# Kernel tuning notes

Hardware: AMD Instinct MI355X
Metric: run time of the kernel (lower is better)

The kernel has to match this reference:

```python
import jax, jax.numpy as jnp
import numpy as np

H = 4        # num_heads
KNN = 10     # k_knn neighbors gathered by distance
KS = 4       # k_select top-k neighbors kept by attention score
EPS = 1e-5
BIG = 1e9


def _ln(x, g, b):
    m = x.mean(-1, keepdims=True)
    v = ((x - m) ** 2).mean(-1, keepdims=True)
    return (x - m) * jax.lax.rsqrt(v + EPS) * g + b


def _sparse_dyn_voxel_attn(x, coords, mask, w_qkv, b_qkv, w_proj, b_proj):
    # x: [B,N,C], coords: [B,N,3], mask: [B,N] bool
    B, N, C = x.shape
    dh = C // H
    qkv = x @ w_qkv + b_qkv                       # [B,N,3C]
    q, k, v = jnp.split(qkv, 3, axis=-1)
    q = q.reshape(B, N, H, dh).transpose(0, 2, 1, 3)   # [B,H,N,dh]
    k = k.reshape(B, N, H, dh).transpose(0, 2, 1, 3)
    v = v.reshape(B, N, H, dh).transpose(0, 2, 1, 3)

    # KNN over voxel coordinates; empty voxels pushed to far distance
    d2 = jnp.sum((coords[:, :, None, :] - coords[:, None, :, :]) ** 2, axis=-1)  # [B,N,N]
    d2 = jnp.where(mask[:, None, :], d2, BIG)
    _, nbr = jax.lax.top_k(-d2, KNN)              # [B,N,KNN] nearest-neighbor indices

    # gather neighbor keys/values: [B,H,N,KNN,dh]
    kn = jax.vmap(lambda a, i: a[:, i, :])(k, nbr)
    vn = jax.vmap(lambda a, i: a[:, i, :])(v, nbr)
    nmask = jax.vmap(lambda m, i: m[i])(mask, nbr)  # [B,N,KNN]

    scale = float(1.0 / np.sqrt(dh))
    scores = jnp.einsum('bhnd,bhnkd->bhnk', q, kn) * scale  # [B,H,N,KNN]
    scores = scores + jnp.where(nmask, 0.0, -BIG)[:, None, :, :]

    # dynamic selection: keep top k_select neighbors by score, softmax over them
    sv, si = jax.lax.top_k(scores, KS)            # [B,H,N,KS]
    w = jax.nn.softmax(sv, axis=-1)
    vsel = jnp.take_along_axis(vn, si[..., None], axis=3)   # [B,H,N,KS,dh]
    o = jnp.einsum('bhnk,bhnkd->bhnd', w, vsel)   # [B,H,N,dh]
    o = o.transpose(0, 2, 1, 3).reshape(B, N, C) @ w_proj + b_proj
    return jnp.where(mask[..., None], o, 0.0)


def setup_inputs() -> dict:
    key = jax.random.key(0)
    ks = jax.random.split(key, 8)
    B, N, C, M = 4, 4096, 64, 256  # N = 16^3 voxels
    s = lambda k, sh: jax.random.normal(k, sh, jnp.float32) * 0.02
    return dict(
        inputs=jax.random.normal(ks[0], (B, N, C), jnp.float32),
        voxel_coords=jax.random.uniform(ks[1], (B, N, 3), jnp.float32) * 16.0,
        non_empty_mask=jax.random.randint(ks[2], (B, N), 0, 2).astype(bool),
        ln1_g=jnp.ones(C, jnp.float32), ln1_b=jnp.zeros(C, jnp.float32),
        ln2_g=jnp.ones(C, jnp.float32), ln2_b=jnp.zeros(C, jnp.float32),
        w_qkv=s(ks[3], (C, 3 * C)), b_qkv=jnp.zeros(3 * C, jnp.float32),
        w_proj=s(ks[4], (C, C)), b_proj=jnp.zeros(C, jnp.float32),
        w1=s(ks[5], (C, M)), b1=jnp.zeros(M, jnp.float32),
        w2=s(ks[6], (M, C)), b2=jnp.zeros(C, jnp.float32),
    )


def reference(inputs, voxel_coords, non_empty_mask, ln1_g, ln1_b, ln2_g, ln2_b,
              w_qkv, b_qkv, w_proj, b_proj, w1, b1, w2, b2):
    a = _sparse_dyn_voxel_attn(_ln(inputs, ln1_g, ln1_b), voxel_coords,
                               non_empty_mask, w_qkv, b_qkv, w_proj, b_proj)
    x = 0.5 * a + inputs                          # drop_path(attn)*0.5 + shortcut (eval)
    h = jax.nn.gelu(_ln(x, ln2_g, ln2_b) @ w1 + b1) @ w2 + b2
    return 0.5 * h + x
```

## Files before the change

### kernel.cpp

```cpp
#include <hip/hip_runtime.h>
#include <hip/hip_bf16.h>
#include <math.h>

#define NH   4
#define DH   16
#define CH   64
#define KNN  10
#define KS   4
#define NV   4096
#define NB   4
#define MHID 256
#define BN   (NB * NV)

#define P_LN1G  0
#define P_LN1B  64
#define P_LN2G  128
#define P_LN2B  192
#define P_WQKV  256
#define P_BQKV  12544
#define P_WPROJ 12736
#define P_BPROJ 16832
#define P_W1    16896
#define P_B1    33280
#define P_W2    33536
#define P_B2    49920
#define P_TOT   49984

#define N_ING  (BN * CH + P_TOT + BN)
#define N_ING4 (N_ING / 4)
#define N_PACK (16384 + 16384 + 12288)
#define NPREP  ((N_ING4 + N_PACK + 255) / 256)

typedef __hip_bfloat16 bf16;
typedef __attribute__((ext_vector_type(8))) short short8;
typedef __attribute__((ext_vector_type(4))) float float4a;
typedef unsigned long long ull;

__device__ __forceinline__ float b2f(bf16 x) { return __bfloat162float(x); }

__device__ __forceinline__ float cvt(const void* p, int i, int isbf) {
  return isbf ? b2f(((const bf16*)p)[i]) : ((const float*)p)[i];
}

__device__ __forceinline__ float us2f(unsigned short u) {
  return __uint_as_float(((unsigned)u) << 16);
}

__device__ __forceinline__ float4 cvt4(const void* p, int i, int isbf) {
  float4 r;
  if (isbf) {
    ushort4 u = *(const ushort4*)((const unsigned short*)p + i);
    r.x = us2f(u.x); r.y = us2f(u.y); r.z = us2f(u.z); r.w = us2f(u.w);
  } else {
    r = *(const float4*)((const float*)p + i);
  }
  return r;
}

__device__ __forceinline__ float wave_sum_f32(float v) {
#pragma unroll
  for (int m = 32; m >= 1; m >>= 1) v += __shfl_xor(v, m, 64);
  return v;
}

__device__ __forceinline__ void wave_min_kv(unsigned& hi, unsigned& lo) {
#pragma unroll
  for (int m = 32; m >= 1; m >>= 1) {
    unsigned ohi = __shfl_xor(hi, m, 64);
    unsigned olo = __shfl_xor(lo, m, 64);
    if (ohi < hi || (ohi == hi && olo < lo)) { hi = ohi; lo = olo; }
  }
}

__device__ __forceinline__ float tanh_fast(float u) {
  float e = __expf(2.0f * u);
  return 1.0f - 2.0f / (e + 1.0f);
}

__device__ __forceinline__ float d2f(float x, float y, float z,
                                     float qx, float qy, float qz) {
  float dx = x - qx, dy = y - qy, dz = z - qz;
  return dx * dx + dy * dy + dz * dz;
}

__device__ __forceinline__ void knn_insert(ull* arr, ull key) {
  if (key < arr[KNN - 1]) {
#pragma unroll
    for (int t = 0; t < KNN; ++t) {
      ull a = arr[t];
      bool lt = key < a;
      ull mn = lt ? key : a;
      ull mx = lt ? a : key;
      arr[t] = mn;
      key = mx;
    }
  }
}

__global__ __launch_bounds__(256) void k_prep(
    const void* xin, const void* coords, const void* maskr,
    const void* ln1g, const void* ln1b, const void* ln2g, const void* ln2b,
    const void* wqkv, const void* bqkv, const void* wproj, const void* bproj,
    const void* w1, const void* b1, const void* w2, const void* b2,
    float* __restrict__ xcan,
    float* __restrict__ pcan, int* __restrict__ mcan,
    unsigned short* __restrict__ w1p, unsigned short* __restrict__ w2p,
    unsigned short* __restrict__ wqp, int* __restrict__ flags)
{
  __shared__ int sfl[2];
  const int tid = threadIdx.x;
  if (tid < 64) {
    const unsigned short* xu = (const unsigned short*)xin;
    const unsigned* mu = (const unsigned*)maskr;
    int c = 0;
#pragma unroll
    for (int k = 0; k < 4; ++k) {
      unsigned short w = xu[tid * 4 + k];
      int e = (w >> 7) & 0xFF;
      c += (e >= 100 && e <= 140);
    }
#pragma unroll
    for (int m = 32; m >= 1; m >>= 1) c += __shfl_xor(c, m, 64);
    unsigned big = (mu[tid] > 1u) ? 1u : 0u;
#pragma unroll
    for (int m = 32; m >= 1; m >>= 1) big |= __shfl_xor(big, m, 64);
    if (tid == 0) {
      sfl[0] = (c >= 205) ? 1 : 0;
      sfl[1] = big ? 1 : 0;
      if (blockIdx.x == 0) { flags[0] = sfl[0]; flags[1] = sfl[1]; }
    }
  }
  __syncthreads();
  const int isbf = sfl[0], m8 = sfl[1];

  int id = blockIdx.x * 256 + tid;
  if (id < N_ING4) {
    int e4 = id * 4;
    const int n0 = BN * CH, n2 = P_TOT;
    if (e4 < n0) { *(float4*)&xcan[e4] = cvt4(xin, e4, isbf); return; }
    e4 -= n0;
    if (e4 < n2) {
      const void* src; int off;
      if      (e4 < P_LN1B)  { src = ln1g;  off = e4 - P_LN1G; }
      else if (e4 < P_LN2G)  { src = ln1b;  off = e4 - P_LN1B; }
      else if (e4 < P_LN2B)  { src = ln2g;  off = e4 - P_LN2G; }
      else if (e4 < P_WQKV)  { src = ln2b;  off = e4 - P_LN2B; }
      else if (e4 < P_BQKV)  { src = wqkv;  off = e4 - P_WQKV; }
      else if (e4 < P_WPROJ) { src = bqkv;  off = e4 - P_BQKV; }
      else if (e4 < P_BPROJ) { src = wproj; off = e4 - P_WPROJ; }
      else if (e4 < P_W1)    { src = bproj; off = e4 - P_BPROJ; }
      else if (e4 < P_B1)    { src = w1;    off = e4 - P_W1; }
      else if (e4 < P_W2)    { src = b1;    off = e4 - P_B1; }
      else if (e4 < P_B2)    { src = w2;    off = e4 - P_W2; }
      else                   { src = b2;    off = e4 - P_B2; }
      *(float4*)&pcan[e4] = cvt4(src, off, isbf);
      return;
    }
    e4 -= n2;
    if (m8) {
      uchar4 u = *(const uchar4*)((const unsigned char*)maskr + e4);
      mcan[e4 + 0] = u.x != 0; mcan[e4 + 1] = u.y != 0;
      mcan[e4 + 2] = u.z != 0; mcan[e4 + 3] = u.w != 0;
    } else {
      int4 vv = *(const int4*)((const int*)maskr + e4);
      mcan[e4 + 0] = vv.x != 0; mcan[e4 + 1] = vv.y != 0;
      mcan[e4 + 2] = vv.z != 0; mcan[e4 + 3] = vv.w != 0;
    }
    return;
  }
  id -= N_ING4;
  if (id < 16384) {
    int j = id & 7, l = (id >> 3) & 63, kh = (id >> 9) & 1, nt = id >> 10;
    int k = kh * 32 + ((l >> 4) * 8) + j;
    int n = nt * 16 + (l & 15);
    w1p[id] = __bfloat16_as_ushort(__float2bfloat16(cvt(w1, k * MHID + n, isbf)));
    return;
  }
  id -= 16384;
  if (id < 16384) {
    int j = id & 7, l = (id >> 3) & 63, kh = (id >> 9) & 7, nt = id >> 12;
    int k = kh * 32 + ((l >> 4) * 8) + j;
    int n = nt * 16 + (l & 15);
    w2p[id] = __bfloat16_as_ushort(__float2bfloat16(cvt(w2, k * CH + n, isbf)));
    return;
  }
  id -= 16384;
  if (id < 12288) {
    int j = id & 7, l = (id >> 3) & 63, kh = (id >> 9) & 1, nt = id >> 10;
    int k = kh * 32 + ((l >> 4) * 8) + j;
    int n = nt * 16 + (l & 15);
    wqp[id] = __bfloat16_as_ushort(__float2bfloat16(cvt(wqkv, k * 192 + n, isbf)));
  }
}

__global__ __launch_bounds__(1024) void k_bin(
    const void* xin, const void* coords, const void* maskr,
    float4* __restrict__ pbin, unsigned* __restrict__ lstart)
{
  __shared__ int sfl[2];
  __shared__ unsigned cnt[16], cur[16];
  const int tid = threadIdx.x;
  if (tid < 64) {
    const unsigned short* xu = (const unsigned short*)xin;
    const unsigned* mu = (const unsigned*)maskr;
    int c = 0;
#pragma unroll
    for (int k = 0; k < 4; ++k) {
      unsigned short w = xu[tid * 4 + k];
      int e = (w >> 7) & 0xFF;
      c += (e >= 100 && e <= 140);
    }
#pragma unroll
    for (int m = 32; m >= 1; m >>= 1) c += __shfl_xor(c, m, 64);
    unsigned big = (mu[tid] > 1u) ? 1u : 0u;
#pragma unroll
    for (int m = 32; m >= 1; m >>= 1) big |= __shfl_xor(big, m, 64);
    if (tid == 0) { sfl[0] = (c >= 205) ? 1 : 0; sfl[1] = big ? 1 : 0; }
  }
  if (tid < 16) { cnt[tid] = 0; }
  __syncthreads();
  const int isbf = sfl[0], m8 = sfl[1];

  const int b = blockIdx.x;
  const unsigned char* m8p = (const unsigned char*)maskr + (size_t)b * NV;
  const int* m32p = (const int*)maskr + (size_t)b * NV;
  unsigned* stg = lstart + b * 17;
  const int lane = tid & 63;
  const ull below = (lane == 0) ? 0ull : (~0ull >> (64 - lane));

  unsigned myc = 0;
#pragma unroll 1
  for (int k = 0; k < 4; ++k) {
    const int j = tid + k * 1024;
    const int mv = m8 ? (m8p[j] != 0) : (m32p[j] != 0);
    int lz = 16;
    if (mv) {
      float z = cvt(coords, (b * NV + j) * 3 + 2, isbf);
      int cz = (int)z; lz = cz > 15 ? 15 : cz;
    }
#pragma unroll
    for (int bb = 0; bb < 16; ++bb) {
      ull m = __ballot(lz == bb);
      if (lane == bb) myc += (unsigned)__popcll(m);
    }
  }
  if (lane < 16) atomicAdd(&cnt[lane], myc);
  __syncthreads();

  if (tid == 0) {
    unsigned run = 0;
#pragma unroll
    for (int bb = 0; bb < 16; ++bb) {
      stg[bb] = run; cur[bb] = run; run += cnt[bb];
    }
    stg[16] = run;
  }
  __syncthreads();

#pragma unroll 1
  for (int k = 0; k < 4; ++k) {
    const int j = tid + k * 1024;
    const int mv = m8 ? (m8p[j] != 0) : (m32p[j] != 0);
    int lz = 16;
    float x = 0.f, y = 0.f, z = 0.f;
    if (mv) {
      int e = (b * NV + j) * 3;
      x = cvt(coords, e, isbf); y = cvt(coords, e + 1, isbf);
      z = cvt(coords, e + 2, isbf);
      int cz = (int)z; lz = cz > 15 ? 15 : cz;
    }
#pragma unroll 1
    for (int bb = 0; bb < 16; ++bb) {
      ull m = __ballot(lz == bb);
      if (m) {
        unsigned base0 = 0;
        if (lane == bb) base0 = atomicAdd(&cur[bb], (unsigned)__popcll(m));
        unsigned base = __shfl(base0, bb, 64);
        if (lz == bb) {
          unsigned pos = base + (unsigned)__popcll(m & below);
          float4 q; q.x = x; q.y = y; q.z = z; q.w = __int_as_float(j);
          pbin[(size_t)b * NV + pos] = q;
        }
      }
    }
  }
}

#define XQS 72
__global__ __launch_bounds__(256) void k_ln_qkv(
    const float* __restrict__ x, const float* __restrict__ pcan,
    const unsigned short* __restrict__ wqp, float* __restrict__ qkv)
{
  __shared__ unsigned short xnb[16 * XQS];
  const int tid = threadIdx.x;
  const int wave = tid >> 6, lane = tid & 63;
  const int row0 = blockIdx.x * 16;

  {
    const float gg = pcan[P_LN1G + lane], bb = pcan[P_LN1B + lane];
#pragma unroll
    for (int r = 0; r < 4; ++r) {
      int m = wave * 4 + r;
      float v = x[(size_t)(row0 + m) * CH + lane];
      float mn = wave_sum_f32(v) * (1.0f / 64.0f);
      float d = v - mn;
      float var = wave_sum_f32(d * d) * (1.0f / 64.0f);
      float rs = 1.0f / sqrtf(var + 1e-5f);
      xnb[m * XQS + lane] =
          __bfloat16_as_ushort(__float2bfloat16(d * rs * gg + bb));
    }
  }
  __syncthreads();

  const int q = lane >> 4, c = lane & 15;
  short8 a0 = *(const short8*)&xnb[c * XQS + q * 8];
  short8 a1 = *(const short8*)&xnb[c * XQS + 32 + q * 8];

#pragma unroll
  for (int t = 0; t < 3; ++t) {
    int nt = wave * 3 + t;
    short8 b0 = *(const short8*)&wqp[(size_t)((nt * 2 + 0) * 64 + lane) * 8];
    short8 b1 = *(const short8*)&wqp[(size_t)((nt * 2 + 1) * 64 + lane) * 8];
    float4a z = {0.f, 0.f, 0.f, 0.f};
    z = __builtin_amdgcn_mfma_f32_16x16x32_bf16(a0, b0, z, 0, 0, 0);
    z = __builtin_amdgcn_mfma_f32_16x16x32_bf16(a1, b1, z, 0, 0, 0);
    int n = nt * 16 + c;
    float bq = pcan[P_BQKV + n];
#pragma unroll
    for (int r = 0; r < 4; ++r) {
      int m = q * 4 + r;
      qkv[(size_t)(row0 + m) * 192 + n] = z[r] + bq;
    }
  }
}

#define CAPK 128
__global__ __launch_bounds__(256) void k_knn5(
    const float4* __restrict__ pbin, const unsigned* __restrict__ lstart,
    int* __restrict__ nbr)
{
  __shared__ ull sb[4][CAPK];
  __shared__ unsigned d9s[4];
  const int wave = threadIdx.x >> 6, lane = threadIdx.x & 63;
  const int b = blockIdx.x >> 10;
  const int slot = (blockIdx.x & 1023) * 4 + wave;
  const unsigned* st = lstart + b * 17;
  const int nval = (int)st[16];
  if (slot >= nval) return;
  const float4* gpt = pbin + (size_t)b * NV;
  ull* kb = sb[wave];
  const ull below = (lane == 0) ? 0ull : (~0ull >> (64 - lane));

  const float4 me = gpt[slot];
  const float qx = me.x, qy = me.y, qz = me.z;
  const int qi = __float_as_int(me.w);
  int cz = (int)qz; cz = cz > 15 ? 15 : cz;
  const int row = (b << 12) | qi;

  int R = 2;
  for (;;) {
    const int zlo = cz - R < 0 ? 0 : cz - R;
    const int zhi = cz + R > 15 ? 15 : cz + R;
    const int s = (int)st[zlo], e = (int)st[zhi + 1];
    const int n = e - s;

    unsigned lm = 0xFFFFFFFFu;
    for (int i = s + lane; i < e; i += 64) {
      float4 p = gpt[i];
      unsigned db = __float_as_uint(d2f(p.x, p.y, p.z, qx, qy, qz));
      lm = db < lm ? db : lm;
    }
    unsigned acc = 0;
#pragma unroll 1
    for (int bit = 31; bit >= 0; --bit) {
      unsigned tr = acc | (1u << bit);
      int c = __popcll(__ballot(lm < tr));
      if (c <= KNN - 1) acc = tr;
    }
    const unsigned T = acc + 8;

    int cnt = 0;
    for (int i0 = 0; i0 < n; i0 += 64) {
      const int i = i0 + lane;
      const int ii = s + (i < n ? i : 0);
      float4 p = gpt[ii];
      unsigned db = __float_as_uint(d2f(p.x, p.y, p.z, qx, qy, qz));
      bool sel = (i < n) && (db <= T);
      ull bal = __ballot(sel);
      if (sel) {
        int pos = cnt + __popcll(bal & below);
        if (pos < CAPK)
          kb[pos] = ((ull)db << 32) | (unsigned)__float_as_int(p.w);
      }
      cnt += __popcll(bal);
    }
    __builtin_amdgcn_wave_barrier();

    unsigned d9bits;
    if (cnt >= KNN && cnt <= CAPK) {
#pragma unroll 1
      for (int o = 0; o < CAPK; o += 64) {
        const int idx = o + lane;
        if (idx < cnt) {
          const ull my = kb[idx];
          int rank = 0;
          for (int i = 0; i < cnt; ++i) rank += (kb[i] < my) ? 1 : 0;
          if (rank < KNN) {
            nbr[(size_t)row * KNN + rank] = (int)(my & (NV - 1));
            if (rank == KNN - 1) d9s[wave] = (unsigned)(my >> 32);
          }
        }
      }
      __builtin_amdgcn_wave_barrier();
      d9bits = d9s[wave];
    } else {
      ull arr[KNN];
#pragma unroll
      for (int t = 0; t < KNN; ++t) arr[t] = ~0ull;
      for (int i = s + lane; i < e; i += 64) {
        float4 p = gpt[i];
        unsigned db = __float_as_uint(d2f(p.x, p.y, p.z, qx, qy, qz));
        knn_insert(arr, ((ull)db << 32) | (unsigned)__float_as_int(p.w));
      }
      unsigned myj = 0;
      d9bits = 0xFFFFFFFFu;
#pragma unroll 1
      for (int r = 0; r < KNN; ++r) {
        unsigned hi = (unsigned)(arr[0] >> 32);
        unsigned lo = (unsigned)(arr[0] & 0xffffffffu);
        wave_min_kv(hi, lo);
        const ull win = ((ull)hi << 32) | lo;
        if (arr[0] == win) {
#pragma unroll
          for (int t = 0; t < KNN - 1; ++t) arr[t] = arr[t + 1];
          arr[KNN - 1] = ~0ull;
        }
        if (lane == r) myj = lo;
        if (r == KNN - 1) d9bits = hi;
      }
      if (lane < KNN) nbr[(size_t)row * KNN + lane] = (int)(myj & (NV - 1));
    }

    const float d9 = __uint_as_float(d9bits);
    if (d9 <= (float)(R * R)) break;
    if (zlo == 0 && zhi == 15) break;
    ++R;
  }
}

#define XNS 72
#define GS  264
__global__ __launch_bounds__(256) void k_attn_mlp(
    const float* __restrict__ qkv, const int* __restrict__ nbr,
    const int* __restrict__ mcan, const float* __restrict__ xcan,
    const float* __restrict__ pcan,
    const unsigned short* __restrict__ w1p,
    const unsigned short* __restrict__ w2p,
    const int* __restrict__ flags, void* __restrict__ out)
{
  __shared__ float wp[CH * CH];
  __shared__ float bp[CH];
  __shared__ float otile[16][CH];
  __shared__ float xtile[16][CH];
  __shared__ float sc[4][NH][KNN];
  __shared__ float wsel[4][NH][KS];
  __shared__ int   isel[4][NH][KS];
  __shared__ int   nb[4][KNN];
  __shared__ float npen[4][KNN];
  __shared__ unsigned short xnb[16 * XNS];
  __shared__ unsigned short gb[16 * GS];
  const int tid = threadIdx.x;
  const int wave = tid >> 6, lane = tid & 63;
  const int row0 = blockIdx.x * 16;
  const int b = row0 / NV;

  {
    const float4* src = (const float4*)(pcan + P_WPROJ);
    float4* dst = (float4*)wp;
    for (int i = tid; i < CH * CH / 4; i += 256) dst[i] = src[i];
    if (tid < CH) bp[tid] = pcan[P_BPROJ + tid];
  }
  __syncthreads();

#pragma unroll 1
  for (int r = 0; r < 4; ++r) {
    const int m = wave * 4 + r;
    const int row = row0 + m;
    if (mcan[row]) {
      if (lane < KNN) {
        int j = nbr[(size_t)row * KNN + lane] & (NV - 1);
        nb[wave][lane] = j;
        npen[wave][lane] = mcan[b * NV + j] ? 0.0f : -1e9f;
      }
      __builtin_amdgcn_wave_barrier();
      if (lane < NH * KNN) {
        int h = lane / KNN, kk = lane % KNN;
        int j = nb[wave][kk];
        const float* qp = qkv + (size_t)row * 192 + h * DH;
        const float* kp = qkv + ((size_t)(b * NV + j)) * 192 + 64 + h * DH;
        float acc = 0.f;
#pragma unroll
        for (int d = 0; d < DH; ++d) acc += qp[d] * kp[d];
        sc[wave][h][kk] = acc * 0.25f + npen[wave][kk];
      }
      __builtin_amdgcn_wave_barrier();
      if (lane < NH) {
        int h = lane;
        float sv[KS]; int sj[KS];
        unsigned used = 0;
#pragma unroll
        for (int rr = 0; rr < KS; ++rr) {
          float best = -INFINITY; int bi = 0;
#pragma unroll
          for (int kk = 0; kk < KNN; ++kk) {
            float s = sc[wave][h][kk];
            if (!(used & (1u << kk)) && s > best) { best = s; bi = kk; }
          }
          used |= 1u << bi; sv[rr] = best; sj[rr] = bi;
        }
        float mx = sv[0];
        float e[KS], sum = 0.f;
#pragma unroll
        for (int rr = 0; rr < KS; ++rr) { e[rr] = expf(sv[rr] - mx); sum += e[rr]; }
        float inv = 1.0f / sum;
#pragma unroll
        for (int rr = 0; rr < KS; ++rr) {
          wsel[wave][h][rr] = e[rr] * inv;
          isel[wave][h][rr] = nb[wave][sj[rr]];
        }
      }
      __builtin_amdgcn_wave_barrier();
      {
        int h = lane >> 4, d = lane & 15;
        float o = 0.f;
#pragma unroll
        for (int rr = 0; rr < KS; ++rr) {
          int j = isel[wave][h][rr];
          o += wsel[wave][h][rr] *
               qkv[((size_t)(b * NV + j)) * 192 + 128 + h * DH + d];
        }
        otile[m][lane] = o;
      }
      __builtin_amdgcn_wave_barrier();
    }
  }

#pragma unroll 1
  for (int r = 0; r < 4; ++r) {
    const int m = wave * 4 + r;
    const int row = row0 + m;
    float x = xcan[(size_t)row * CH + lane];
    if (mcan[row]) {
      float acc = bp[lane];
#pragma unroll 4
      for (int cc = 0; cc < CH; ++cc)
        acc = fmaf(otile[m][cc], wp[cc * CH + lane], acc);
      x += 0.5f * acc;
    }
    xtile[m][lane] = x;
  }

  {
    const float gg = pcan[P_LN2G + lane], bb2 = pcan[P_LN2B + lane];
#pragma unroll
    for (int r = 0; r < 4; ++r) {
      int m = wave * 4 + r;
      float v = xtile[m][lane];
      float mn = wave_sum_f32(v) * (1.0f / 64.0f);
      float d = v - mn;
      float var = wave_sum_f32(d * d) * (1.0f / 64.0f);
      float rs = 1.0f / sqrtf(var + 1e-5f);
      xnb[m * XNS + lane] =
          __bfloat16_as_ushort(__float2bfloat16(d * rs * gg + bb2));
    }
  }
  __syncthreads();

  const int q = lane >> 4, c = lane & 15;
  short8 a0 = *(const short8*)&xnb[c * XNS + q * 8];
  short8 a1 = *(const short8*)&xnb[c * XNS + 32 + q * 8];

  float4a acc1[4];
#pragma unroll
  for (int t = 0; t < 4; ++t) {
    int nt = wave * 4 + t;
    short8 b0 = *(const short8*)&w1p[(size_t)((nt * 2 + 0) * 64 + lane) * 8];
    short8 b1 = *(const short8*)&w1p[(size_t)((nt * 2 + 1) * 64 + lane) * 8];
    float4a z = {0.f, 0.f, 0.f, 0.f};
    z = __builtin_amdgcn_mfma_f32_16x16x32_bf16(a0, b0, z, 0, 0, 0);
    z = __builtin_amdgcn_mfma_f32_16x16x32_bf16(a1, b1, z, 0, 0, 0);
    acc1[t] = z;
  }
#pragma unroll
  for (int t = 0; t < 4; ++t) {
    int n = (wave * 4 + t) * 16 + c;
    float bo = pcan[P_B1 + n];
#pragma unroll
    for (int r = 0; r < 4; ++r) {
      float h = acc1[t][r] + bo;
      float u = 0.7978845608028654f * (h + 0.044715f * h * h * h);
      float gv = 0.5f * h * (1.0f + tanh_fast(u));
      gb[(q * 4 + r) * GS + n] = __bfloat16_as_ushort(__float2bfloat16(gv));
    }
  }
  __syncthreads();

  float4a o = {0.f, 0.f, 0.f, 0.f};
#pragma unroll
  for (int kh = 0; kh < 8; ++kh) {
    short8 ag = *(const short8*)&gb[c * GS + kh * 32 + q * 8];
    short8 bg = *(const short8*)&w2p[(size_t)((wave * 8 + kh) * 64 + lane) * 8];
    o = __builtin_amdgcn_mfma_f32_16x16x32_bf16(ag, bg, o, 0, 0, 0);
  }
  {
    int n = wave * 16 + c;
    float b2v = pcan[P_B2 + n];
    const int isbf = flags[0];
#pragma unroll
    for (int r = 0; r < 4; ++r) {
      int m = q * 4 + r;
      size_t idx = (size_t)(row0 + m) * CH + n;
      float val = 0.5f * (o[r] + b2v) + xtile[m][n];
      if (isbf) ((bf16*)out)[idx] = __float2bfloat16(val);
      else      ((float*)out)[idx] = val;
    }
  }
}

extern "C" void kernel_launch(void* const* d_in, const int* in_sizes, int n_in,
                              void* d_out, int out_size, void* d_ws, size_t ws_size,
                              hipStream_t stream)
{
  char* ws = (char*)d_ws;
  float* qkv   = (float*)(ws);
  float* xcan  = (float*)(ws + 16777216);
  float* pcan  = (float*)(ws + 21168128);
  int*   mcan  = (int*)  (ws + 21368064);
  int*   nbr   = (int*)  (ws + 21433600);
  int*   flags = (int*)  (ws + 22088960);
  unsigned short* w1p = (unsigned short*)(ws + 22089728);
  unsigned short* w2p = (unsigned short*)(ws + 22122496);
  unsigned short* wqp = (unsigned short*)(ws + 22155264);
  float4*   pbin   = (float4*)  (ws + 22179840);
  unsigned* lstart = (unsigned*)(ws + 22441984);

  k_prep<<<NPREP, 256, 0, stream>>>(
      d_in[0], d_in[1], d_in[2], d_in[3], d_in[4], d_in[5], d_in[6],
      d_in[7], d_in[8], d_in[9], d_in[10], d_in[11], d_in[12], d_in[13], d_in[14],
      xcan, pcan, mcan, w1p, w2p, wqp, flags);
  k_bin<<<NB, 1024, 0, stream>>>(d_in[0], d_in[1], d_in[2], pbin, lstart);
  k_ln_qkv<<<BN / 16, 256, 0, stream>>>(xcan, pcan, wqp, qkv);
  k_knn5<<<NB * (NV / 4), 256, 0, stream>>>(pbin, lstart, nbr);
  k_attn_mlp<<<BN / 16, 256, 0, stream>>>(qkv, nbr, mcan, xcan, pcan,
                                          w1p, w2p, flags, d_out);
}
```

Measured before the change: 154.2 us.

## Merge binning into LN-QKV launch and make KNN search incremental over slabs

The z-binning kernel is folded into the LN+QKV kernel as extra leading blocks of 256 threads, which removes one launch. The KNN kernel drops the threshold/shared-buffer rank selection. It now keeps per-lane top-10 register lists and expands the z-slab radius incrementally, scanning only the newly added slabs instead of rescanning the whole window each time. The trade-off is that binning now runs with a quarter of the threads per batch, and insertion-sort work per candidate replaces the cheaper threshold filter.

```diff
diff --git a/kernel.cpp b/kernel.cpp
--- a/kernel.cpp
+++ b/kernel.cpp
@@ -58,6 +58,12 @@
 }
 
 __device__ __forceinline__ float wave_sum_f32(float v) {
+#pragma unroll
+  for (int m = 32; m >= 1; m >>= 1) v += __shfl_xor(v, m, 64);
+  return v;
+}
+
+__device__ __forceinline__ int wave_sum_i32(int v) {
 #pragma unroll
   for (int m = 32; m >= 1; m >>= 1) v += __shfl_xor(v, m, 64);
   return v;
@@ -193,109 +199,107 @@
   }
 }
 
-__global__ __launch_bounds__(1024) void k_bin(
+#define XQS 72
+__global__ __launch_bounds__(256) void k_mid(
     const void* xin, const void* coords, const void* maskr,
-    float4* __restrict__ pbin, unsigned* __restrict__ lstart)
-{
-  __shared__ int sfl[2];
-  __shared__ unsigned cnt[16], cur[16];
-  const int tid = threadIdx.x;
-  if (tid < 64) {
-    const unsigned short* xu = (const unsigned short*)xin;
-    const unsigned* mu = (const unsigned*)maskr;
-    int c = 0;
-#pragma unroll
-    for (int k = 0; k < 4; ++k) {
-      unsigned short w = xu[tid * 4 + k];
-      int e = (w >> 7) & 0xFF;
-      c += (e >= 100 && e <= 140);
-    }
-#pragma unroll
-    for (int m = 32; m >= 1; m >>= 1) c += __shfl_xor(c, m, 64);
-    unsigned big = (mu[tid] > 1u) ? 1u : 0u;
-#pragma unroll
-    for (int m = 32; m >= 1; m >>= 1) big |= __shfl_xor(big, m, 64);
-    if (tid == 0) { sfl[0] = (c >= 205) ? 1 : 0; sfl[1] = big ? 1 : 0; }
-  }
-  if (tid < 16) { cnt[tid] = 0; }
-  __syncthreads();
-  const int isbf = sfl[0], m8 = sfl[1];
-
-  const int b = blockIdx.x;
-  const unsigned char* m8p = (const unsigned char*)maskr + (size_t)b * NV;
-  const int* m32p = (const int*)maskr + (size_t)b * NV;
-  unsigned* stg = lstart + b * 17;
-  const int lane = tid & 63;
-  const ull below = (lane == 0) ? 0ull : (~0ull >> (64 - lane));
-
-  unsigned myc = 0;
-#pragma unroll 1
-  for (int k = 0; k < 4; ++k) {
-    const int j = tid + k * 1024;
-    const int mv = m8 ? (m8p[j] != 0) : (m32p[j] != 0);
-    int lz = 16;
-    if (mv) {
-      float z = cvt(coords, (b * NV + j) * 3 + 2, isbf);
-      int cz = (int)z; lz = cz > 15 ? 15 : cz;
-    }
-#pragma unroll
-    for (int bb = 0; bb < 16; ++bb) {
-      ull m = __ballot(lz == bb);
-      if (lane == bb) myc += (unsigned)__popcll(m);
-    }
-  }
-  if (lane < 16) atomicAdd(&cnt[lane], myc);
-  __syncthreads();
-
-  if (tid == 0) {
-    unsigned run = 0;
-#pragma unroll
-    for (int bb = 0; bb < 16; ++bb) {
-      stg[bb] = run; cur[bb] = run; run += cnt[bb];
-    }
-    stg[16] = run;
-  }
-  __syncthreads();
-
-#pragma unroll 1
-  for (int k = 0; k < 4; ++k) {
-    const int j = tid + k * 1024;
-    const int mv = m8 ? (m8p[j] != 0) : (m32p[j] != 0);
-    int lz = 16;
-    float x = 0.f, y = 0.f, z = 0.f;
-    if (mv) {
-      int e = (b * NV + j) * 3;
-      x = cvt(coords, e, isbf); y = cvt(coords, e + 1, isbf);
-      z = cvt(coords, e + 2, isbf);
-      int cz = (int)z; lz = cz > 15 ? 15 : cz;
-    }
-#pragma unroll 1
-    for (int bb = 0; bb < 16; ++bb) {
-      ull m = __ballot(lz == bb);
-      if (m) {
-        unsigned base0 = 0;
-        if (lane == bb) base0 = atomicAdd(&cur[bb], (unsigned)__popcll(m));
-        unsigned base = __shfl(base0, bb, 64);
-        if (lz == bb) {
-          unsigned pos = base + (unsigned)__popcll(m & below);
-          float4 q; q.x = x; q.y = y; q.z = z; q.w = __int_as_float(j);
-          pbin[(size_t)b * NV + pos] = q;
-        }
-      }
-    }
-  }
-}
-
-#define XQS 72
-__global__ __launch_bounds__(256) void k_ln_qkv(
+    float4* __restrict__ pbin, unsigned* __restrict__ lstart,
     const float* __restrict__ x, const float* __restrict__ pcan,
     const unsigned short* __restrict__ wqp, float* __restrict__ qkv)
 {
   __shared__ unsigned short xnb[16 * XQS];
+  __shared__ int sfl[2];
+  __shared__ unsigned cnt[16], cur[16];
   const int tid = threadIdx.x;
   const int wave = tid >> 6, lane = tid & 63;
-  const int row0 = blockIdx.x * 16;
-
+
+  if (blockIdx.x < NB) {
+    if (tid < 64) {
+      const unsigned short* xu = (const unsigned short*)xin;
+      const unsigned* mu = (const unsigned*)maskr;
+      int c = 0;
+#pragma unroll
+      for (int k = 0; k < 4; ++k) {
+        unsigned short w = xu[tid * 4 + k];
+        int e = (w >> 7) & 0xFF;
+        c += (e >= 100 && e <= 140);
+      }
+#pragma unroll
+      for (int m = 32; m >= 1; m >>= 1) c += __shfl_xor(c, m, 64);
+      unsigned big = (mu[tid] > 1u) ? 1u : 0u;
+#pragma unroll
+      for (int m = 32; m >= 1; m >>= 1) big |= __shfl_xor(big, m, 64);
+      if (tid == 0) { sfl[0] = (c >= 205) ? 1 : 0; sfl[1] = big ? 1 : 0; }
+    }
+    if (tid < 16) cnt[tid] = 0;
+    __syncthreads();
+    const int isbf = sfl[0], m8 = sfl[1];
+
+    const int b = blockIdx.x;
+    const unsigned char* m8p = (const unsigned char*)maskr + (size_t)b * NV;
+    const int* m32p = (const int*)maskr + (size_t)b * NV;
+    unsigned* stg = lstart + b * 17;
+    const ull below = (lane == 0) ? 0ull : (~0ull >> (64 - lane));
+
+    unsigned myc = 0;
+#pragma unroll 1
+    for (int k = 0; k < 16; ++k) {
+      const int j = tid + k * 256;
+      const int mv = m8 ? (m8p[j] != 0) : (m32p[j] != 0);
+      int lz = 16;
+      if (mv) {
+        float z = cvt(coords, (b * NV + j) * 3 + 2, isbf);
+        int cz = (int)z; lz = cz > 15 ? 15 : cz;
+      }
+#pragma unroll
+      for (int bb = 0; bb < 16; ++bb) {
+        ull m = __ballot(lz == bb);
+        if (lane == bb) myc += (unsigned)__popcll(m);
+      }
+    }
+    if (lane < 16) atomicAdd(&cnt[lane], myc);
+    __syncthreads();
+
+    if (tid == 0) {
+      unsigned run = 0;
+#pragma unroll
+      for (int bb = 0; bb < 16; ++bb) {
+        stg[bb] = run; cur[bb] = run; run += cnt[bb];
+      }
+      stg[16] = run;
+    }
+    __syncthreads();
+
+#pragma unroll 1
+    for (int k = 0; k < 16; ++k) {
+      const int j = tid + k * 256;
+      const int mv = m8 ? (m8p[j] != 0) : (m32p[j] != 0);
+      int lz = 16;
+      float xx = 0.f, yy = 0.f, zz = 0.f;
+      if (mv) {
+        int e = (b * NV + j) * 3;
+        xx = cvt(coords, e, isbf); yy = cvt(coords, e + 1, isbf);
+        zz = cvt(coords, e + 2, isbf);
+        int cz = (int)zz; lz = cz > 15 ? 15 : cz;
+      }
+#pragma unroll 1
+      for (int bb = 0; bb < 16; ++bb) {
+        ull m = __ballot(lz == bb);
+        if (m) {
+          unsigned base0 = 0;
+          if (lane == bb) base0 = atomicAdd(&cur[bb], (unsigned)__popcll(m));
+          unsigned base = __shfl(base0, bb, 64);
+          if (lz == bb) {
+            unsigned pos = base + (unsigned)__popcll(m & below);
+            float4 q; q.x = xx; q.y = yy; q.z = zz; q.w = __int_as_float(j);
+            pbin[(size_t)b * NV + pos] = q;
+          }
+        }
+      }
+    }
+    return;
+  }
+
+  const int row0 = (blockIdx.x - NB) * 16;
   {
     const float gg = pcan[P_LN1G + lane], bb = pcan[P_LN1B + lane];
 #pragma unroll
@@ -334,13 +338,10 @@
   }
 }
 
-#define CAPK 128
-__global__ __launch_bounds__(256) void k_knn5(
+__global__ __launch_bounds__(256) void k_knn4(
     const float4* __restrict__ pbin, const unsigned* __restrict__ lstart,
     int* __restrict__ nbr)
 {
-  __shared__ ull sb[4][CAPK];
-  __shared__ unsigned d9s[4];
   const int wave = threadIdx.x >> 6, lane = threadIdx.x & 63;
   const int b = blockIdx.x >> 10;
   const int slot = (blockIdx.x & 1023) * 4 + wave;
@@ -348,104 +349,80 @@
   const int nval = (int)st[16];
   if (slot >= nval) return;
   const float4* gpt = pbin + (size_t)b * NV;
-  ull* kb = sb[wave];
-  const ull below = (lane == 0) ? 0ull : (~0ull >> (64 - lane));
 
   const float4 me = gpt[slot];
   const float qx = me.x, qy = me.y, qz = me.z;
   const int qi = __float_as_int(me.w);
   int cz = (int)qz; cz = cz > 15 ? 15 : cz;
-  const int row = (b << 12) | qi;
+
+  ull arr[KNN];
+#pragma unroll
+  for (int t = 0; t < KNN; ++t) arr[t] = ~0ull;
 
   int R = 2;
-  for (;;) {
-    const int zlo = cz - R < 0 ? 0 : cz - R;
-    const int zhi = cz + R > 15 ? 15 : cz + R;
+  int zlo = cz - 2 < 0 ? 0 : cz - 2;
+  int zhi = cz + 2 > 15 ? 15 : cz + 2;
+  {
     const int s = (int)st[zlo], e = (int)st[zhi + 1];
-    const int n = e - s;
-
-    unsigned lm = 0xFFFFFFFFu;
     for (int i = s + lane; i < e; i += 64) {
       float4 p = gpt[i];
-      unsigned db = __float_as_uint(d2f(p.x, p.y, p.z, qx, qy, qz));
-      lm = db < lm ? db : lm;
-    }
-    unsigned acc = 0;
-#pragma unroll 1
-    for (int bit = 31; bit >= 0; --bit) {
-      unsigned tr = acc | (1u << bit);
-      int c = __popcll(__ballot(lm < tr));
-      if (c <= KNN - 1) acc = tr;
-    }
-    const unsigned T = acc + 8;
-
-    int cnt = 0;
-    for (int i0 = 0; i0 < n; i0 += 64) {
-      const int i = i0 + lane;
-      const int ii = s + (i < n ? i : 0);
-      float4 p = gpt[ii];
-      unsigned db = __float_as_uint(d2f(p.x, p.y, p.z, qx, qy, qz));
-      bool sel = (i < n) && (db <= T);
-      ull bal = __ballot(sel);
-      if (sel) {
-        int pos = cnt + __popcll(bal & below);
-        if (pos < CAPK)
-          kb[pos] = ((ull)db << 32) | (unsigned)__float_as_int(p.w);
-      }
-      cnt += __popcll(bal);
-    }
-    __builtin_amdgcn_wave_barrier();
-
-    unsigned d9bits;
-    if (cnt >= KNN && cnt <= CAPK) {
-#pragma unroll 1
-      for (int o = 0; o < CAPK; o += 64) {
-        const int idx = o + lane;
-        if (idx < cnt) {
-          const ull my = kb[idx];
-          int rank = 0;
-          for (int i = 0; i < cnt; ++i) rank += (kb[i] < my) ? 1 : 0;
-          if (rank < KNN) {
-            nbr[(size_t)row * KNN + rank] = (int)(my & (NV - 1));
-            if (rank == KNN - 1) d9s[wave] = (unsigned)(my >> 32);
-          }
-        }
-      }
-      __builtin_amdgcn_wave_barrier();
-      d9bits = d9s[wave];
-    } else {
-      ull arr[KNN];
-#pragma unroll
-      for (int t = 0; t < KNN; ++t) arr[t] = ~0ull;
+      float d2 = d2f(p.x, p.y, p.z, qx, qy, qz);
+      knn_insert(arr, ((ull)__float_as_uint(d2) << 32) |
+                      (unsigned)__float_as_int(p.w));
+    }
+  }
+
+  for (;;) {
+    const float RR = (float)(R * R);
+    int c = 0;
+#pragma unroll
+    for (int t = 0; t < KNN; ++t) {
+      float d = __uint_as_float((unsigned)(arr[t] >> 32));
+      c += (d <= RR) ? 1 : 0;
+    }
+    c = wave_sum_i32(c);
+    if (c >= KNN) break;
+    if (zlo == 0 && zhi == 15) break;
+    ++R;
+    const int nzlo = cz - R < 0 ? 0 : cz - R;
+    const int nzhi = cz + R > 15 ? 15 : cz + R;
+    {
+      const int s = (int)st[nzlo], e = (int)st[zlo];
       for (int i = s + lane; i < e; i += 64) {
         float4 p = gpt[i];
-        unsigned db = __float_as_uint(d2f(p.x, p.y, p.z, qx, qy, qz));
-        knn_insert(arr, ((ull)db << 32) | (unsigned)__float_as_int(p.w));
-      }
-      unsigned myj = 0;
-      d9bits = 0xFFFFFFFFu;
+        float d2 = d2f(p.x, p.y, p.z, qx, qy, qz);
+        knn_insert(arr, ((ull)__float_as_uint(d2) << 32) |
+                        (unsigned)__float_as_int(p.w));
+      }
+    }
+    {
+      const int s = (int)st[zhi + 1], e = (int)st[nzhi + 1];
+      for (int i = s + lane; i < e; i += 64) {
+        float4 p = gpt[i];
+        float d2 = d2f(p.x, p.y, p.z, qx, qy, qz);
+        knn_insert(arr, ((ull)__float_as_uint(d2) << 32) |
+                        (unsigned)__float_as_int(p.w));
+      }
+    }
+    zlo = nzlo; zhi = nzhi;
+  }
+
+  unsigned myj = 0;
 #pragma unroll 1
-      for (int r = 0; r < KNN; ++r) {
-        unsigned hi = (unsigned)(arr[0] >> 32);
-        unsigned lo = (unsigned)(arr[0] & 0xffffffffu);
-        wave_min_kv(hi, lo);
-        const ull win = ((ull)hi << 32) | lo;
-        if (arr[0] == win) {
-#pragma unroll
-          for (int t = 0; t < KNN - 1; ++t) arr[t] = arr[t + 1];
-          arr[KNN - 1] = ~0ull;
-        }
-        if (lane == r) myj = lo;
-        if (r == KNN - 1) d9bits = hi;
-      }
-      if (lane < KNN) nbr[(size_t)row * KNN + lane] = (int)(myj & (NV - 1));
-    }
-
-    const float d9 = __uint_as_float(d9bits);
-    if (d9 <= (float)(R * R)) break;
-    if (zlo == 0 && zhi == 15) break;
-    ++R;
-  }
+  for (int r = 0; r < KNN; ++r) {
+    unsigned hi = (unsigned)(arr[0] >> 32);
+    unsigned lo = (unsigned)(arr[0] & 0xffffffffu);
+    wave_min_kv(hi, lo);
+    const ull win = ((ull)hi << 32) | lo;
+    if (arr[0] == win) {
+#pragma unroll
+      for (int t = 0; t < KNN - 1; ++t) arr[t] = arr[t + 1];
+      arr[KNN - 1] = ~0ull;
+    }
+    if (lane == r) myj = lo;
+  }
+  const int row = (b << 12) | qi;
+  if (lane < KNN) nbr[(size_t)row * KNN + lane] = (int)(myj & (NV - 1));
 }
 
 #define XNS 72
@@ -648,9 +625,9 @@
       d_in[0], d_in[1], d_in[2], d_in[3], d_in[4], d_in[5], d_in[6],
       d_in[7], d_in[8], d_in[9], d_in[10], d_in[11], d_in[12], d_in[13], d_in[14],
       xcan, pcan, mcan, w1p, w2p, wqp, flags);
-  k_bin<<<NB, 1024, 0, stream>>>(d_in[0], d_in[1], d_in[2], pbin, lstart);
-  k_ln_qkv<<<BN / 16, 256, 0, stream>>>(xcan, pcan, wqp, qkv);
-  k_knn5<<<NB * (NV / 4), 256, 0, stream>>>(pbin, lstart, nbr);
+  k_mid<<<NB + BN / 16, 256, 0, stream>>>(d_in[0], d_in[1], d_in[2],
+                                          pbin, lstart, xcan, pcan, wqp, qkv);
+  k_knn4<<<NB * (NV / 4), 256, 0, stream>>>(pbin, lstart, nbr);
   k_attn_mlp<<<BN / 16, 256, 0, stream>>>(qkv, nbr, mcan, xcan, pcan,
                                           w1p, w2p, flags, d_out);
 }
```

Result: slower. 189.3 us (+22.7%).
